# Kernel optimization log

Measured on AMD Instinct MI355X. Metric: run time of the kernel, lower is better.

Reference implementation:

```python
import jax, jax.numpy as jnp
import numpy as np

B, C, D = 4, 1024, 1024
H, DH = 16, 64  # num_heads, head_size; D == H*DH


def setup_inputs() -> dict:
    key = jax.random.key(0)
    ks = jax.random.split(key, 8)
    return {
        "query_input": jax.random.normal(ks[0], (B, C, D), dtype=jnp.float32),
        "key_input": jax.random.normal(ks[1], (B, C, D), dtype=jnp.float32),
        "value_input": jax.random.normal(ks[2], (B, C, D), dtype=jnp.float32),
        "Wq": jax.random.normal(ks[3], (D, D), dtype=jnp.float32) * 0.02,
        "Wk": jax.random.normal(ks[4], (D, D), dtype=jnp.float32) * 0.02,
        "Wv": jax.random.normal(ks[5], (D, D), dtype=jnp.float32) * 0.02,
        "Wp": jax.random.normal(ks[6], (D, D), dtype=jnp.float32) * 0.02,
        "bp": jax.random.normal(ks[7], (D,), dtype=jnp.float32) * 0.02,
        "mask": jnp.zeros((C, C), dtype=bool),
    }


def _split_heads(x):
    # (B, C, D) -> (B, H, C, DH)
    return x.reshape(B, C, H, DH).transpose(0, 2, 1, 3)


def reference(query_input, key_input, value_input, Wq, Wk, Wv, Wp, bp, mask):
    scale = DH ** -0.5
    q = _split_heads(query_input @ Wq.T)
    k = _split_heads(key_input @ Wk.T)
    v = _split_heads(value_input @ Wv.T)
    # ||q_i - k_j||_2 via norm decomposition: |q|^2 + |k|^2 - 2 q.k
    q2 = jnp.sum(q * q, axis=-1)  # (B, H, C)
    k2 = jnp.sum(k * k, axis=-1)  # (B, H, C)
    qk = jnp.einsum("bhqd,bhkd->bhqk", q, k)  # (B, H, C, C)
    sq = jnp.maximum(q2[..., :, None] + k2[..., None, :] - 2.0 * qk, 0.0)
    wei = jnp.sqrt(sq) * scale
    wei = jnp.where(mask, -jnp.inf, wei)
    wei = jax.nn.softmax(wei, axis=-1)
    out = jnp.einsum("bhqk,bhkd->bhqd", wei, v)  # (B, H, C, DH)
    out = out.transpose(0, 2, 1, 3).reshape(B, C, D)
    return out @ Wp.T + bp
```

## Files before the change

kernel.cpp:

```cpp
#include <hip/hip_runtime.h>


typedef _Float16 f16;
typedef __attribute__((ext_vector_type(2))) _Float16 f16x2;
typedef __attribute__((ext_vector_type(8))) _Float16 f16x8;
typedef __attribute__((ext_vector_type(4))) float f32x4;
typedef __attribute__((ext_vector_type(16))) float f32x16;

#define MFMA16(a, b, c) __builtin_amdgcn_mfma_f32_16x16x32_f16((a), (b), (c), 0, 0, 0)
#define MFMA32(a, b, c) __builtin_amdgcn_mfma_f32_32x32x16_f16((a), (b), (c), 0, 0, 0)

constexpr double LOG2E = 1.4426950408889634;
constexpr double C2d = 0.015625 * LOG2E * LOG2E;

#if __has_builtin(__builtin_amdgcn_exp2f)
#define EXP2F(x) __builtin_amdgcn_exp2f(x)
#else
#define EXP2F(x) exp2f(x)
#endif
#if __has_builtin(__builtin_amdgcn_sqrtf)
#define SQRTF(x) __builtin_amdgcn_sqrtf(x)
#else
#define SQRTF(x) sqrtf(x)
#endif

__device__ __forceinline__ void stage16(const void* g, void* lds_base_uniform) {
#if __has_builtin(__builtin_amdgcn_global_load_lds)
    __builtin_amdgcn_global_load_lds((const __attribute__((address_space(1))) void*)g,
                                     (__attribute__((address_space(3))) void*)lds_base_uniform,
                                     16, 0, 0);
#else
    const int lane = threadIdx.x & 63;
    *(f16x8*)((f16*)lds_base_uniform + lane * 8) = *(const f16x8*)g;
#endif
}

__device__ __forceinline__ f16x8 cvt8v(f32x4 a, f32x4 b) {
    f16x8 o;
    o[0] = (f16)a[0]; o[1] = (f16)a[1]; o[2] = (f16)a[2]; o[3] = (f16)a[3];
    o[4] = (f16)b[0]; o[5] = (f16)b[1]; o[6] = (f16)b[2]; o[7] = (f16)b[3];
    return o;
}

__global__ __launch_bounds__(256) void cvt_all(const float* __restrict__ Xq,
                                               const float* __restrict__ Xk,
                                               const float* __restrict__ Xv,
                                               const float* __restrict__ Wq,
                                               const float* __restrict__ Wk,
                                               const float* __restrict__ Wv,
                                               const float* __restrict__ Wp,
                                               f16* __restrict__ W16,
                                               f16* __restrict__ X16) {
    const size_t idx = (size_t)blockIdx.x * 2048 + threadIdx.x * 8;
    const size_t M4 = 4ull << 20, M1 = 1ull << 20;
    const float* s;
    f16* d;
    if (idx < 3 * M4) {
        if (idx < M4) s = Xq + idx;
        else if (idx < 2 * M4) s = Xk + (idx - M4);
        else s = Xv + (idx - 2 * M4);
        d = X16 + idx;
    } else {
        size_t wi = idx - 3 * M4;
        if (wi < M1) s = Wq + wi;
        else if (wi < 2 * M1) s = Wk + (wi - M1);
        else if (wi < 3 * M1) s = Wv + (wi - 2 * M1);
        else s = Wp + (wi - 3 * M1);
        d = W16 + wi;
    }
    f32x4 a = *(const f32x4*)s;
    f32x4 b = *(const f32x4*)(s + 4);
    *(f16x8*)d = cvt8v(a, b);
}

template <bool NORMS, bool F32OUT>
__device__ __forceinline__ void gemm128(f16* As, f16* Bs,
                                        const f16* __restrict__ Ap,
                                        const f16* __restrict__ Bp,
                                        f16* __restrict__ Cop,
                                        float* __restrict__ Cf,
                                        const float* __restrict__ bias,
                                        float* __restrict__ nrmp,
                                        float osc, float nscale,
                                        int row0, int col0, int N, int K) {
    const int tid = threadIdx.x;
    const int lane = tid & 63;
    const int w = tid >> 6;
    const int l31 = lane & 31, l5 = lane >> 5;
    const int wr = (w >> 1) * 64, wc = (w & 1) * 64;

    f32x16 acc[2][2] = {};

    for (int kt = 0; kt < K; kt += 64) {
        __syncthreads();
#pragma unroll
        for (int t = 0; t < 4; ++t) {
            const int rb = w * 32 + t * 8;
            const int rr = rb + (lane >> 3);
            const int gs = (lane & 7) ^ (rr & 7);
            stage16(&Ap[(size_t)(row0 + rr) * K + kt + gs * 8], &As[rb * 64]);
            stage16(&Bp[(size_t)(col0 + rr) * K + kt + gs * 8], &Bs[rb * 64]);
        }
        __syncthreads();
#pragma unroll
        for (int ks = 0; ks < 4; ++ks) {
            const int gq = ks * 2 + l5;
            f16x8 af[2], bf[2];
#pragma unroll
            for (int mr = 0; mr < 2; ++mr)
                af[mr] = *(const f16x8*)&As[(wr + mr * 32 + l31) * 64 + ((gq ^ (l31 & 7)) * 8)];
#pragma unroll
            for (int n2 = 0; n2 < 2; ++n2)
                bf[n2] = *(const f16x8*)&Bs[(wc + n2 * 32 + l31) * 64 + ((gq ^ (l31 & 7)) * 8)];
#pragma unroll
            for (int mr = 0; mr < 2; ++mr)
#pragma unroll
                for (int n2 = 0; n2 < 2; ++n2) acc[mr][n2] = MFMA32(af[mr], bf[n2], acc[mr][n2]);
        }
    }

    const int cc0 = col0 + wc + l31;
    const int cc1 = col0 + wc + 32 + l31;
    const int hh = (col0 + wc) >> 6;
#pragma unroll
    for (int mr = 0; mr < 2; ++mr)
#pragma unroll
        for (int j = 0; j < 16; ++j) {
            const int rr = row0 + wr + mr * 32 + (j & 3) + 8 * (j >> 2) + 4 * l5;
            if (F32OUT) {
                Cf[(size_t)rr * N + cc0] = acc[mr][0][j] + bias[cc0];
                Cf[(size_t)rr * N + cc1] = acc[mr][1][j] + bias[cc1];
            } else {
                const f16 h0 = (f16)(acc[mr][0][j] * osc);
                const f16 h1 = (f16)(acc[mr][1][j] * osc);
                if (NORMS) {
                    float v0 = (float)h0, v1 = (float)h1;
                    float s = v0 * v0 + v1 * v1;
                    s += __shfl_xor(s, 1);
                    s += __shfl_xor(s, 2);
                    s += __shfl_xor(s, 4);
                    s += __shfl_xor(s, 8);
                    s += __shfl_xor(s, 16);
                    if (l31 == 0)
                        nrmp[(size_t)((rr >> 10) * 16 + hh) * 1024 + (rr & 1023)] = s * nscale;
                }
                Cop[(size_t)rr * N + cc0] = h0;
                Cop[(size_t)rr * N + cc1] = h1;
            }
        }
}

__global__ __launch_bounds__(256, 2) void gemm_qkv(const f16* __restrict__ X16,
                                                   const f16* __restrict__ W16,
                                                   f16* __restrict__ qb_base,
                                                   f16* __restrict__ vTb,
                                                   float* __restrict__ nrm,
                                                   float qsc, float ns_q, float ns_k) {
    __shared__ __attribute__((aligned(16))) f16 As[128 * 64];
    __shared__ __attribute__((aligned(16))) f16 Bs[128 * 64];
    const int bid = blockIdx.x;
    if (bid < 512) {
        const int z = bid >> 8;
        const int f = bid & 255;
        const int g = (f & 7) * 32 + (f >> 3);
        const int row0 = (g >> 3) * 128, col0 = (g & 7) * 128;
        gemm128<true, false>(As, Bs,
                             X16 + (size_t)z * (4u << 20), W16 + (size_t)z * (1u << 20),
                             qb_base + (size_t)z * (4u << 20), nullptr, nullptr,
                             nrm + (size_t)z * 65536,
                             z ? 1.0f : qsc, z ? ns_k : ns_q, row0, col0, 1024, 1024);
    } else {
        const int f = bid - 512;
        const int g = (f & 7) * 32 + (f >> 3);
        const int row0 = (g >> 5) * 128, col0 = (g & 31) * 128;
        gemm128<false, false>(As, Bs,
                              W16 + 2 * (1u << 20), X16 + 2 * (4u << 20),
                              vTb, nullptr, nullptr, nullptr,
                              1.0f, 0.f, row0, col0, 4096, 1024);
    }
}

__global__ __launch_bounds__(256, 2) void gemm_fin(const f16* __restrict__ A,
                                                   const f16* __restrict__ B,
                                                   float* __restrict__ Cf,
                                                   const float* __restrict__ bias) {
    __shared__ __attribute__((aligned(16))) f16 As[64 * 64];
    __shared__ __attribute__((aligned(16))) f16 Bs[128 * 64];
    const int tid = threadIdx.x;
    const int lane = tid & 63;
    const int w = tid >> 6;
    const int l31 = lane & 31, l5 = lane >> 5;
    const int wr = (w & 1) * 32, wc = (w >> 1) * 64;
    const int f = blockIdx.x;
    const int g = (f & 7) * 64 + (f >> 3);
    const int row0 = (g >> 3) * 64, col0 = (g & 7) * 128;
    const int K = 1024, N = 1024;

    f32x16 acc[2] = {};

    for (int kt = 0; kt < K; kt += 64) {
        __syncthreads();
#pragma unroll
        for (int t = 0; t < 2; ++t) {
            const int rb = w * 16 + t * 8;
            const int rr = rb + (lane >> 3);
            const int gs = (lane & 7) ^ (rr & 7);
            stage16(&A[(size_t)(row0 + rr) * K + kt + gs * 8], &As[rb * 64]);
        }
#pragma unroll
        for (int t = 0; t < 4; ++t) {
            const int rb = w * 32 + t * 8;
            const int rr = rb + (lane >> 3);
            const int gs = (lane & 7) ^ (rr & 7);
            stage16(&B[(size_t)(col0 + rr) * K + kt + gs * 8], &Bs[rb * 64]);
        }
        __syncthreads();
#pragma unroll
        for (int ks = 0; ks < 4; ++ks) {
            const int gq = ks * 2 + l5;
            f16x8 af = *(const f16x8*)&As[(wr + l31) * 64 + ((gq ^ (l31 & 7)) * 8)];
#pragma unroll
            for (int n2 = 0; n2 < 2; ++n2) {
                f16x8 bf = *(const f16x8*)&Bs[(wc + n2 * 32 + l31) * 64 + ((gq ^ (l31 & 7)) * 8)];
                acc[n2] = MFMA32(af, bf, acc[n2]);
            }
        }
    }

    const int cc0 = col0 + wc + l31;
    const int cc1 = col0 + wc + 32 + l31;
#pragma unroll
    for (int j = 0; j < 16; ++j) {
        const int rr = row0 + wr + (j & 3) + 8 * (j >> 2) + 4 * l5;
        Cf[(size_t)rr * N + cc0] = acc[0][j] + bias[cc0];
        Cf[(size_t)rr * N + cc1] = acc[1][j] + bias[cc1];
    }
}

__global__ __launch_bounds__(512, 2) void attn(const f16* __restrict__ qs,
                                               const f16* __restrict__ kb,
                                               const f16* __restrict__ vT,
                                               const float* __restrict__ q2c2,
                                               const float* __restrict__ k2c2,
                                               f16* __restrict__ out) {
    __shared__ __attribute__((aligned(16))) char smem[67 * 1024];
    f16* KsA = (f16*)smem;
    f16* VsA = (f16*)(smem + 32768);
    float* k2tA = (float*)(smem + 65536);
    float* mbuf = (float*)smem;

    const int tid = threadIdx.x;
    const int grp = tid >> 8;
    const int t2 = tid & 255;
    const int lane = tid & 63;
    const int w4 = t2 >> 6;
    const int l15 = lane & 15, l4 = lane >> 4;
    f16* Ks = KsA + grp * (128 * 64);
    f16* Vs = VsA + grp * (64 * 128);
    float* k2t = k2tA + grp * 128;

    const int fid = blockIdx.y * 8 + blockIdx.x;
    const int qt = (fid >> 3) & 7;
    const int bh = (fid & 7) * 8 + (fid >> 6);
    const int b = bh >> 4, h = bh & 15;
    const int wq = w4 * 32;
    const int hcol = h * 64;
    const int qrow0 = b * 1024 + qt * 128;
    const f16* vTh = vT + (size_t)hcol * 4096 + b * 1024;

    const int sr = t2 >> 3, sc0 = (t2 & 7) * 8;
    const int vr = t2 >> 4, vc0 = (t2 & 15) * 8;
    const int vsw = (vr & 7) << 3;
    const int fsw = (l15 & 7) << 3;

    f16x8 bq[2][2];
#pragma unroll
    for (int m = 0; m < 2; ++m)
#pragma unroll
        for (int ks = 0; ks < 2; ++ks)
            bq[m][ks] = *(const f16x8*)&qs[(size_t)(qrow0 + wq + m * 16 + l15) * 1024 + hcol + ks * 32 + l4 * 8];
    float q2m[2];
#pragma unroll
    for (int m = 0; m < 2; ++m) q2m[m] = q2c2[(size_t)bh * 1024 + qt * 128 + wq + m * 16 + l15];

    f32x4 accv[2][4] = {};
    f32x4 dacc[2] = {};
    const f16 one = (f16)1.f;
    const f16x8 ones8 = {one, one, one, one, one, one, one, one};

    f16x8 kreg[4], vreg[4];
    float k2reg = 0.f;
#define ISSUE_LOADS(KT)                                                                                      \
    {                                                                                                        \
        _Pragma("unroll") for (int i = 0; i < 4; ++i)                                                        \
            kreg[i] = *(const f16x8*)&kb[(size_t)(b * 1024 + (KT) * 128 + sr + i * 32) * 1024 + hcol + sc0]; \
        _Pragma("unroll") for (int j = 0; j < 4; ++j)                                                        \
            vreg[j] = *(const f16x8*)&vTh[(size_t)(vr + j * 16) * 4096 + (KT) * 128 + vc0];                  \
        k2reg = (t2 < 128) ? k2c2[(size_t)bh * 1024 + (KT) * 128 + t2] : 0.f;                                \
    }

    ISSUE_LOADS(grp * 4)

    for (int ktl = 0; ktl < 4; ++ktl) {
        __syncthreads();
#pragma unroll
        for (int i = 0; i < 4; ++i) {
            const int kap = sr + i * 32;
            const int s = ((kap >> 5) & 3) * 32 + ((kap >> 2) & 1) * 16 + ((kap >> 3) & 3) * 4 + (kap & 3);
            *(f16x8*)&Ks[s * 64 + (sc0 ^ ((s & 7) << 3))] = kreg[i];
        }
#pragma unroll
        for (int j = 0; j < 4; ++j) *(f16x8*)&Vs[(vr + j * 16) * 128 + (vc0 ^ vsw)] = vreg[j];
        if (t2 < 128) k2t[t2] = k2reg;
        __syncthreads();
        if (ktl < 3) ISSUE_LOADS(grp * 4 + ktl + 1)

#pragma unroll
        for (int kk = 0; kk < 4; ++kk) {
            unsigned um[2][4];
#pragma unroll
            for (int half = 0; half < 2; ++half) {
                const int n = kk * 2 + half;
                f16x8 kf0 = *(const f16x8*)&Ks[(n * 16 + l15) * 64 + ((l4 * 8) ^ fsw)];
                f16x8 kf1 = *(const f16x8*)&Ks[(n * 16 + l15) * 64 + ((32 + l4 * 8) ^ fsw)];
                f32x4 k2q = *(const f32x4*)&k2t[kk * 32 + l4 * 8 + half * 4];
#pragma unroll
                for (int m = 0; m < 2; ++m) {
                    f32x4 c0;
#pragma unroll
                    for (int r = 0; r < 4; ++r) c0[r] = q2m[m] + k2q[r];
                    f32x4 st = MFMA16(kf0, bq[m][0], c0);
                    st = MFMA16(kf1, bq[m][1], st);
                    float p0 = EXP2F(SQRTF(fmaxf(st[0], 0.f)));
                    float p1 = EXP2F(SQRTF(fmaxf(st[1], 0.f)));
                    float p2 = EXP2F(SQRTF(fmaxf(st[2], 0.f)));
                    float p3 = EXP2F(SQRTF(fmaxf(st[3], 0.f)));
                    f16x2 lo = {(f16)p0, (f16)p1};
                    f16x2 hi = {(f16)p2, (f16)p3};
                    um[m][half * 2] = __builtin_bit_cast(unsigned, lo);
                    um[m][half * 2 + 1] = __builtin_bit_cast(unsigned, hi);
                }
            }
            f16x8 ap[2];
#pragma unroll
            for (int m = 0; m < 2; ++m) {
                uint4 u = {um[m][0], um[m][1], um[m][2], um[m][3]};
                ap[m] = __builtin_bit_cast(f16x8, u);
            }
            __builtin_amdgcn_s_setprio(1);
#pragma unroll
            for (int m = 0; m < 2; ++m) dacc[m] = MFMA16(ap[m], ones8, dacc[m]);
#pragma unroll
            for (int n2 = 0; n2 < 4; ++n2) {
                f16x8 bv = *(const f16x8*)&Vs[(n2 * 16 + l15) * 128 + ((kk * 32 + l4 * 8) ^ fsw)];
#pragma unroll
                for (int m = 0; m < 2; ++m) accv[m][n2] = MFMA16(ap[m], bv, accv[m][n2]);
            }
            __builtin_amdgcn_s_setprio(0);
        }
    }

    __syncthreads();
    if (grp) {
        float* p = mbuf + t2 * 40;
#pragma unroll
        for (int m = 0; m < 2; ++m)
#pragma unroll
            for (int n2 = 0; n2 < 4; ++n2) *(f32x4*)(p + (m * 4 + n2) * 4) = accv[m][n2];
        *(f32x4*)(p + 32) = dacc[0];
        *(f32x4*)(p + 36) = dacc[1];
    }
    __syncthreads();
    if (!grp) {
        float* p = mbuf + t2 * 40;
#pragma unroll
        for (int m = 0; m < 2; ++m)
#pragma unroll
            for (int n2 = 0; n2 < 4; ++n2) accv[m][n2] += *(const f32x4*)(p + (m * 4 + n2) * 4);
        dacc[0] += *(const f32x4*)(p + 32);
        dacc[1] += *(const f32x4*)(p + 36);
#pragma unroll
        for (int m = 0; m < 2; ++m)
#pragma unroll
            for (int r = 0; r < 4; ++r) {
                const float rd = 1.0f / dacc[m][r];
#pragma unroll
                for (int n2 = 0; n2 < 4; ++n2)
                    out[(size_t)(qrow0 + wq + m * 16 + l4 * 4 + r) * 1024 + hcol + n2 * 16 + l15] =
                        (f16)(accv[m][n2][r] * rd);
            }
    }
}

extern "C" void kernel_launch(void* const* d_in, const int* in_sizes, int n_in,
                              void* d_out, int out_size, void* d_ws, size_t ws_size,
                              hipStream_t stream) {
    const float* Xq = (const float*)d_in[0];
    const float* Xk = (const float*)d_in[1];
    const float* Xv = (const float*)d_in[2];
    const float* Wq = (const float*)d_in[3];
    const float* Wk = (const float*)d_in[4];
    const float* Wv = (const float*)d_in[5];
    const float* Wp = (const float*)d_in[6];
    const float* bp = (const float*)d_in[7];
    float* out = (float*)d_out;

    char* ws = (char*)d_ws;
    f16* W16 = (f16*)(ws);
    f16* X16 = (f16*)(ws + (8ull << 20));
    f16* qb = (f16*)(ws + (32ull << 20));
    f16* kb = (f16*)(ws + (40ull << 20));
    f16* vTb = (f16*)(ws + (48ull << 20));
    f16* attnout = (f16*)(ws + (56ull << 20));
    (void)kb;
    float* q2c2 = out;
    float* k2c2 = out + 65536;

    const float qsc = (float)(-2.0 * C2d);
    const float ns_q = (float)(1.0 / (4.0 * C2d));
    const float ns_k = (float)C2d;

    cvt_all<<<8192, 256, 0, stream>>>(Xq, Xk, Xv, Wq, Wk, Wv, Wp, W16, X16);

    gemm_qkv<<<768, 256, 0, stream>>>(X16, W16, qb, vTb, q2c2, qsc, ns_q, ns_k);

    attn<<<dim3(8, 64), 512, 0, stream>>>(qb, kb, vTb, q2c2, k2c2, attnout);

    gemm_fin<<<512, 256, 0, stream>>>(attnout, W16 + 3 * (1u << 20), out, bp);
}
```

Measured before the change: 105.7 us.

## Replace split-KV attention blocks with smaller single-pass query tiles

The attention kernel drops the two-group split over the key dimension and the shared-memory merge of partial results. Each block now has 256 threads and covers 64 query rows, with one 16-row m-tile per wave, and walks all 8 key tiles itself. The grid doubles to 1024 blocks and shared memory per block shrinks to about 33KB. This removes the reduction step and its syncs and raises block count, but K/V tiles are now loaded once per 64 query rows instead of once per 128, adding global traffic. It also loses the per-wave reuse of K and V fragments across two m-tiles and drops the setprio hints.

```diff
diff --git a/kernel.cpp b/kernel.cpp
--- a/kernel.cpp
+++ b/kernel.cpp
@@ -237,54 +237,41 @@
     }
 }
 
-__global__ __launch_bounds__(512, 2) void attn(const f16* __restrict__ qs,
+__global__ __launch_bounds__(256, 2) void attn(const f16* __restrict__ qs,
                                                const f16* __restrict__ kb,
                                                const f16* __restrict__ vT,
                                                const float* __restrict__ q2c2,
                                                const float* __restrict__ k2c2,
                                                f16* __restrict__ out) {
-    __shared__ __attribute__((aligned(16))) char smem[67 * 1024];
-    f16* KsA = (f16*)smem;
-    f16* VsA = (f16*)(smem + 32768);
-    float* k2tA = (float*)(smem + 65536);
-    float* mbuf = (float*)smem;
-
+    __shared__ __attribute__((aligned(16))) f16 Ks[128 * 64];
+    __shared__ __attribute__((aligned(16))) f16 Vs[64 * 128];
+    __shared__ float k2tile[128];
     const int tid = threadIdx.x;
-    const int grp = tid >> 8;
-    const int t2 = tid & 255;
     const int lane = tid & 63;
-    const int w4 = t2 >> 6;
+    const int w = tid >> 6;
     const int l15 = lane & 15, l4 = lane >> 4;
-    f16* Ks = KsA + grp * (128 * 64);
-    f16* Vs = VsA + grp * (64 * 128);
-    float* k2t = k2tA + grp * 128;
-
-    const int fid = blockIdx.y * 8 + blockIdx.x;
-    const int qt = (fid >> 3) & 7;
-    const int bh = (fid & 7) * 8 + (fid >> 6);
+    const int fid = blockIdx.y * 16 + blockIdx.x;
+    const int qt = (fid >> 3) & 15;
+    const int bh = (fid & 7) * 8 + (fid >> 7);
     const int b = bh >> 4, h = bh & 15;
-    const int wq = w4 * 32;
+    const int wq = w * 16;
     const int hcol = h * 64;
-    const int qrow0 = b * 1024 + qt * 128;
+    const int qrow0 = b * 1024 + qt * 64;
     const f16* vTh = vT + (size_t)hcol * 4096 + b * 1024;
 
-    const int sr = t2 >> 3, sc0 = (t2 & 7) * 8;
-    const int vr = t2 >> 4, vc0 = (t2 & 15) * 8;
+    const int sr = tid >> 3, sc0 = (tid & 7) * 8;
+    const int vr = tid >> 4, vc0 = (tid & 15) * 8;
     const int vsw = (vr & 7) << 3;
     const int fsw = (l15 & 7) << 3;
 
-    f16x8 bq[2][2];
-#pragma unroll
-    for (int m = 0; m < 2; ++m)
-#pragma unroll
-        for (int ks = 0; ks < 2; ++ks)
-            bq[m][ks] = *(const f16x8*)&qs[(size_t)(qrow0 + wq + m * 16 + l15) * 1024 + hcol + ks * 32 + l4 * 8];
-    float q2m[2];
-#pragma unroll
-    for (int m = 0; m < 2; ++m) q2m[m] = q2c2[(size_t)bh * 1024 + qt * 128 + wq + m * 16 + l15];
-
-    f32x4 accv[2][4] = {};
-    f32x4 dacc[2] = {};
+    f16x8 bq[2];
+#pragma unroll
+    for (int ks = 0; ks < 2; ++ks)
+        bq[ks] = *(const f16x8*)&qs[(size_t)(qrow0 + wq + l15) * 1024 + hcol + ks * 32 + l4 * 8];
+    const float q2m = q2c2[(size_t)bh * 1024 + qt * 64 + wq + l15];
+
+    f32x4 accv[4] = {};
+    f32x4 dacc = {};
     const f16 one = (f16)1.f;
     const f16x8 ones8 = {one, one, one, one, one, one, one, one};
 
@@ -296,12 +283,12 @@
             kreg[i] = *(const f16x8*)&kb[(size_t)(b * 1024 + (KT) * 128 + sr + i * 32) * 1024 + hcol + sc0]; \
         _Pragma("unroll") for (int j = 0; j < 4; ++j)                                                        \
             vreg[j] = *(const f16x8*)&vTh[(size_t)(vr + j * 16) * 4096 + (KT) * 128 + vc0];                  \
-        k2reg = (t2 < 128) ? k2c2[(size_t)bh * 1024 + (KT) * 128 + t2] : 0.f;                                \
-    }
-
-    ISSUE_LOADS(grp * 4)
-
-    for (int ktl = 0; ktl < 4; ++ktl) {
+        k2reg = (tid < 128) ? k2c2[(size_t)bh * 1024 + (KT) * 128 + tid] : 0.f;                              \
+    }
+
+    ISSUE_LOADS(0)
+
+    for (int kt = 0; kt < 8; ++kt) {
         __syncthreads();
 #pragma unroll
         for (int i = 0; i < 4; ++i) {
@@ -311,84 +298,51 @@
         }
 #pragma unroll
         for (int j = 0; j < 4; ++j) *(f16x8*)&Vs[(vr + j * 16) * 128 + (vc0 ^ vsw)] = vreg[j];
-        if (t2 < 128) k2t[t2] = k2reg;
-        __syncthreads();
-        if (ktl < 3) ISSUE_LOADS(grp * 4 + ktl + 1)
+        if (tid < 128) k2tile[tid] = k2reg;
+        __syncthreads();
+        if (kt < 7) ISSUE_LOADS(kt + 1)
 
 #pragma unroll
         for (int kk = 0; kk < 4; ++kk) {
-            unsigned um[2][4];
+            unsigned um[4];
 #pragma unroll
             for (int half = 0; half < 2; ++half) {
                 const int n = kk * 2 + half;
                 f16x8 kf0 = *(const f16x8*)&Ks[(n * 16 + l15) * 64 + ((l4 * 8) ^ fsw)];
                 f16x8 kf1 = *(const f16x8*)&Ks[(n * 16 + l15) * 64 + ((32 + l4 * 8) ^ fsw)];
-                f32x4 k2q = *(const f32x4*)&k2t[kk * 32 + l4 * 8 + half * 4];
-#pragma unroll
-                for (int m = 0; m < 2; ++m) {
-                    f32x4 c0;
-#pragma unroll
-                    for (int r = 0; r < 4; ++r) c0[r] = q2m[m] + k2q[r];
-                    f32x4 st = MFMA16(kf0, bq[m][0], c0);
-                    st = MFMA16(kf1, bq[m][1], st);
-                    float p0 = EXP2F(SQRTF(fmaxf(st[0], 0.f)));
-                    float p1 = EXP2F(SQRTF(fmaxf(st[1], 0.f)));
-                    float p2 = EXP2F(SQRTF(fmaxf(st[2], 0.f)));
-                    float p3 = EXP2F(SQRTF(fmaxf(st[3], 0.f)));
-                    f16x2 lo = {(f16)p0, (f16)p1};
-                    f16x2 hi = {(f16)p2, (f16)p3};
-                    um[m][half * 2] = __builtin_bit_cast(unsigned, lo);
-                    um[m][half * 2 + 1] = __builtin_bit_cast(unsigned, hi);
-                }
+                f32x4 k2q = *(const f32x4*)&k2tile[kk * 32 + l4 * 8 + half * 4];
+                f32x4 c0;
+#pragma unroll
+                for (int r = 0; r < 4; ++r) c0[r] = q2m + k2q[r];
+                f32x4 st = MFMA16(kf0, bq[0], c0);
+                st = MFMA16(kf1, bq[1], st);
+                float p0 = EXP2F(SQRTF(fmaxf(st[0], 0.f)));
+                float p1 = EXP2F(SQRTF(fmaxf(st[1], 0.f)));
+                float p2 = EXP2F(SQRTF(fmaxf(st[2], 0.f)));
+                float p3 = EXP2F(SQRTF(fmaxf(st[3], 0.f)));
+                f16x2 lo = {(f16)p0, (f16)p1};
+                f16x2 hi = {(f16)p2, (f16)p3};
+                um[half * 2] = __builtin_bit_cast(unsigned, lo);
+                um[half * 2 + 1] = __builtin_bit_cast(unsigned, hi);
             }
-            f16x8 ap[2];
-#pragma unroll
-            for (int m = 0; m < 2; ++m) {
-                uint4 u = {um[m][0], um[m][1], um[m][2], um[m][3]};
-                ap[m] = __builtin_bit_cast(f16x8, u);
-            }
-            __builtin_amdgcn_s_setprio(1);
-#pragma unroll
-            for (int m = 0; m < 2; ++m) dacc[m] = MFMA16(ap[m], ones8, dacc[m]);
+            uint4 u = {um[0], um[1], um[2], um[3]};
+            f16x8 ap = __builtin_bit_cast(f16x8, u);
+            dacc = MFMA16(ap, ones8, dacc);
 #pragma unroll
             for (int n2 = 0; n2 < 4; ++n2) {
                 f16x8 bv = *(const f16x8*)&Vs[(n2 * 16 + l15) * 128 + ((kk * 32 + l4 * 8) ^ fsw)];
-#pragma unroll
-                for (int m = 0; m < 2; ++m) accv[m][n2] = MFMA16(ap[m], bv, accv[m][n2]);
+                accv[n2] = MFMA16(ap, bv, accv[n2]);
             }
-            __builtin_amdgcn_s_setprio(0);
-        }
-    }
-
-    __syncthreads();
-    if (grp) {
-        float* p = mbuf + t2 * 40;
-#pragma unroll
-        for (int m = 0; m < 2; ++m)
-#pragma unroll
-            for (int n2 = 0; n2 < 4; ++n2) *(f32x4*)(p + (m * 4 + n2) * 4) = accv[m][n2];
-        *(f32x4*)(p + 32) = dacc[0];
-        *(f32x4*)(p + 36) = dacc[1];
-    }
-    __syncthreads();
-    if (!grp) {
-        float* p = mbuf + t2 * 40;
-#pragma unroll
-        for (int m = 0; m < 2; ++m)
-#pragma unroll
-            for (int n2 = 0; n2 < 4; ++n2) accv[m][n2] += *(const f32x4*)(p + (m * 4 + n2) * 4);
-        dacc[0] += *(const f32x4*)(p + 32);
-        dacc[1] += *(const f32x4*)(p + 36);
-#pragma unroll
-        for (int m = 0; m < 2; ++m)
-#pragma unroll
-            for (int r = 0; r < 4; ++r) {
-                const float rd = 1.0f / dacc[m][r];
-#pragma unroll
-                for (int n2 = 0; n2 < 4; ++n2)
-                    out[(size_t)(qrow0 + wq + m * 16 + l4 * 4 + r) * 1024 + hcol + n2 * 16 + l15] =
-                        (f16)(accv[m][n2][r] * rd);
-            }
+        }
+    }
+
+#pragma unroll
+    for (int r = 0; r < 4; ++r) {
+        const float rd = 1.0f / dacc[r];
+#pragma unroll
+        for (int n2 = 0; n2 < 4; ++n2)
+            out[(size_t)(qrow0 + wq + l4 * 4 + r) * 1024 + hcol + n2 * 16 + l15] =
+                (f16)(accv[n2][r] * rd);
     }
 }
 
@@ -424,7 +378,7 @@
 
     gemm_qkv<<<768, 256, 0, stream>>>(X16, W16, qb, vTb, q2c2, qsc, ns_q, ns_k);
 
-    attn<<<dim3(8, 64), 512, 0, stream>>>(qb, kb, vTb, q2c2, k2c2, attnout);
+    attn<<<dim3(16, 64), 256, 0, stream>>>(qb, kb, vTb, q2c2, k2c2, attnout);
 
     gemm_fin<<<512, 256, 0, stream>>>(attnout, W16 + 3 * (1u << 20), out, bp);
 }
```

Result: no change. 103.9 us (-1.8%).
